# Kernel tuning notes

Measured on AMD Instinct MI355X. Metric: run time of the kernel, lower is better.

## Reference

```python
import jax, jax.numpy as jnp
import numpy as np

EPS = 1e-5
NUM_HEADS = 16
HEAD_DIM = 64


def layernorm(x, g, b):
    mu = jnp.mean(x, axis=-1, keepdims=True)
    var = jnp.mean(jnp.square(x - mu), axis=-1, keepdims=True)
    return (x - mu) * jax.lax.rsqrt(var + EPS) * g + b


def setup_inputs() -> dict:
    key = jax.random.key(0)
    ks = jax.random.split(key, 10)
    B, S, Q, D = 4, 4096, 256, 1024
    x = jax.random.normal(ks[0], (B, S, D), dtype=jnp.float32)
    queries = jax.random.normal(ks[1], (B, Q, D), dtype=jnp.float32)
    attn_mask = jax.random.randint(ks[2], (B, NUM_HEADS, Q, S), 0, 2) == 1
    key_padding_mask = jax.random.randint(ks[3], (B, S), 0, 2) == 1
    scale = 1.0 / np.sqrt(2.0 * D)  # xavier-ish
    Wq = jax.random.normal(ks[4], (D, D), dtype=jnp.float32) * scale
    Wk = jax.random.normal(ks[5], (D, D), dtype=jnp.float32) * scale
    Wv = jax.random.normal(ks[6], (D, D), dtype=jnp.float32) * scale
    Wo = jax.random.normal(ks[7], (D, D), dtype=jnp.float32) * scale
    ln1_g = jnp.ones((D,), jnp.float32); ln1_b = jnp.zeros((D,), jnp.float32)
    ln2_g = jnp.ones((D,), jnp.float32); ln2_b = jnp.zeros((D,), jnp.float32)
    return {"x": x, "queries": queries, "attn_mask": attn_mask,
            "key_padding_mask": key_padding_mask, "Wq": Wq, "Wk": Wk,
            "Wv": Wv, "Wo": Wo, "ln1_g": ln1_g, "ln1_b": ln1_b,
            "ln2_g": ln2_g, "ln2_b": ln2_b}


def reference(x, queries, attn_mask, key_padding_mask, Wq, Wk, Wv, Wo,
              ln1_g, ln1_b, ln2_g, ln2_b):
    B, S, D = x.shape
    Q = queries.shape[1]
    H, hd = NUM_HEADS, HEAD_DIM

    xn = layernorm(x, ln1_g, ln1_b)
    q = (queries @ Wq.T).reshape(B, Q, H, hd)
    k = (xn @ Wk.T).reshape(B, S, H, hd)
    v = (xn @ Wv.T).reshape(B, S, H, hd)

    # scores: (B, H, Q, S)
    scores = jnp.einsum('bqhd,bshd->bhqs', q, k) / np.sqrt(hd)

    mask = attn_mask | key_padding_mask[:, None, None, :]
    neg_inf = jnp.float32(-jnp.inf)
    masked = jnp.where(mask, neg_inf, scores)
    all_masked = jnp.all(mask, axis=-1, keepdims=True)  # rows fully masked
    safe = jnp.where(all_masked, 0.0, masked)
    attn = jax.nn.softmax(safe, axis=-1)
    attn = jnp.where(all_masked, 0.0, attn)

    out = jnp.einsum('bhqs,bshd->bqhd', attn, v).reshape(B, Q, D)
    out = layernorm(out, ln2_g, ln2_b)
    return out @ Wo.T, attn.mean(axis=1)
```

## Files before the change

### kernel.cpp

```cpp
#include <hip/hip_runtime.h>
#include <math.h>

#define DEV __device__ __forceinline__

typedef float  f4v  __attribute__((ext_vector_type(4)));
typedef __bf16 b8v  __attribute__((ext_vector_type(8)));
typedef short  s8v  __attribute__((ext_vector_type(8)));

DEV short f2b(float f){ __bf16 h = (__bf16)f; return __builtin_bit_cast(short, h); }
DEV float b2f(short s){ __bf16 h = __builtin_bit_cast(__bf16, s); return (float)h; }

DEV void gload16(const void* g, void* l){
  __builtin_amdgcn_global_load_lds((const __attribute__((address_space(1))) void*)g,
                                   (__attribute__((address_space(3))) void*)l, 16, 0, 0);
}

DEV b8v ldsf(const short* p){ return __builtin_bit_cast(b8v, *(const s8v*)p); }

DEV f4v mfma16(b8v a, b8v b, f4v c){ return __builtin_amdgcn_mfma_f32_16x16x32_bf16(a, b, c, 0, 0, 0); }

DEV void lds_barrier(){
  asm volatile("s_waitcnt lgkmcnt(0)" ::: "memory");
  __builtin_amdgcn_s_barrier();
}

__global__ __launch_bounds__(256) void prep_kernel(const float* __restrict__ x, const float* __restrict__ ln1g,
                                                   const float* __restrict__ ln1b, short* __restrict__ xn,
                                                   const float* __restrict__ s0, const float* __restrict__ s1,
                                                   const float* __restrict__ s2, const float* __restrict__ s3,
                                                   const float* __restrict__ s4,
                                                   short* __restrict__ d0, short* __restrict__ d1,
                                                   short* __restrict__ d2, short* __restrict__ d3,
                                                   short* __restrict__ d4){
  int bid = blockIdx.x, tid = threadIdx.x;
  if (bid < 5120){
    int i = bid*256 + tid;
    int buf = i >> 18, j = i & 262143;
    const float* s = (buf==0)?s0:(buf==1)?s1:(buf==2)?s2:(buf==3)?s3:s4;
    short*       d = (buf==0)?d0:(buf==1)?d1:(buf==2)?d2:(buf==3)?d3:d4;
    float4 v = ((const float4*)s)[j];
    ((short4*)d)[j] = make_short4(f2b(v.x), f2b(v.y), f2b(v.z), f2b(v.w));
    return;
  }
  int row = bid - 5120;
  const float4 v = ((const float4*)(x + (size_t)row*1024))[tid];
  float s = v.x + v.y + v.z + v.w;
  #pragma unroll
  for (int off=1; off<64; off<<=1) s += __shfl_xor(s, off);
  __shared__ float red[4];
  if ((tid&63)==0) red[tid>>6] = s;
  __syncthreads();
  float mu = (red[0]+red[1]+red[2]+red[3]) * (1.0f/1024.0f);
  float e0=v.x-mu, e1=v.y-mu, e2=v.z-mu, e3=v.w-mu;
  float q = e0*e0 + e1*e1 + e2*e2 + e3*e3;
  #pragma unroll
  for (int off=1; off<64; off<<=1) q += __shfl_xor(q, off);
  __syncthreads();
  if ((tid&63)==0) red[tid>>6] = q;
  __syncthreads();
  float rs = rsqrtf((red[0]+red[1]+red[2]+red[3]) * (1.0f/1024.0f) + 1e-5f);
  float4 g4 = ((const float4*)ln1g)[tid];
  float4 b4 = ((const float4*)ln1b)[tid];
  short4 o = make_short4(f2b(e0*rs*g4.x + b4.x), f2b(e1*rs*g4.y + b4.y),
                         f2b(e2*rs*g4.z + b4.z), f2b(e3*rs*g4.w + b4.w));
  ((short4*)(xn + (size_t)row*1024))[tid] = o;
}

__global__ __launch_bounds__(256) void ln_reduce_kernel(const short* __restrict__ opart, const float* __restrict__ gg,
                                                        const float* __restrict__ bb, short* __restrict__ out){
  int row = blockIdx.x, tid = threadIdx.x;
  float a0=0.f, a1=0.f, a2=0.f, a3=0.f;
  #pragma unroll
  for (int sc=0; sc<16; ++sc){
    short4 t = ((const short4*)(opart + ((size_t)sc*1024 + row)*1024))[tid];
    a0 += b2f(t.x); a1 += b2f(t.y); a2 += b2f(t.z); a3 += b2f(t.w);
  }
  float s = a0 + a1 + a2 + a3;
  #pragma unroll
  for (int off=1; off<64; off<<=1) s += __shfl_xor(s, off);
  __shared__ float red[4];
  if ((tid&63)==0) red[tid>>6] = s;
  __syncthreads();
  float mu = (red[0]+red[1]+red[2]+red[3]) * (1.0f/1024.0f);
  float d0=a0-mu, d1=a1-mu, d2=a2-mu, d3=a3-mu;
  float q = d0*d0 + d1*d1 + d2*d2 + d3*d3;
  #pragma unroll
  for (int off=1; off<64; off<<=1) q += __shfl_xor(q, off);
  __syncthreads();
  if ((tid&63)==0) red[tid>>6] = q;
  __syncthreads();
  float rs = rsqrtf((red[0]+red[1]+red[2]+red[3]) * (1.0f/1024.0f) + 1e-5f);
  float4 g4 = ((const float4*)gg)[tid];
  float4 b4 = ((const float4*)bb)[tid];
  short4 o = make_short4(f2b(d0*rs*g4.x + b4.x), f2b(d1*rs*g4.y + b4.y),
                         f2b(d2*rs*g4.z + b4.z), f2b(d3*rs*g4.w + b4.w));
  ((short4*)(out + (size_t)row*1024))[tid] = o;
}

template<int OUTF32>
__global__ __launch_bounds__(256) void gemm_small(const short* __restrict__ A, const short* __restrict__ B,
                                                  void* __restrict__ C, int M, int N, int K){
  __shared__ short sA[2][64*64];
  __shared__ short sB[2][64*64];
  int tid=threadIdx.x, lane=tid&63, wv=tid>>6, g=lane>>4, r=lane&15;
  int wr=wv>>1, wc=wv&1;
  int m0=blockIdx.x*64, n0=blockIdx.y*64;
  f4v z = {0.f,0.f,0.f,0.f};
  f4v acc[2][2];
  #pragma unroll
  for (int i=0;i<2;++i){
    #pragma unroll
    for (int j=0;j<2;++j) acc[i][j]=z;
  }
  auto stage = [&](int buf, int kt){
    #pragma unroll
    for (int i=0;i<2;++i){
      int idx = i*256 + tid;
      int row = idx>>3, cbs = (idx&7)^(row&7);
      gload16(A + (size_t)(m0+row)*K + kt*64 + cbs*8, &sA[buf][(i*256+wv*64)*8]);
      gload16(B + (size_t)(n0+row)*K + kt*64 + cbs*8, &sB[buf][(i*256+wv*64)*8]);
    }
  };
  int nkt = K >> 6;
  stage(0, 0);
  __syncthreads();
  for (int kt=0; kt<nkt; ++kt){
    int cur = kt & 1;
    if (kt+1 < nkt) stage(cur^1, kt+1);
    b8v af[2][2], bf[2][2];
    #pragma unroll
    for (int mf=0;mf<2;++mf){
      #pragma unroll
      for (int ks=0;ks<2;++ks){
        int ra = wr*32 + mf*16 + r;
        int rb = wc*32 + mf*16 + r;
        af[mf][ks] = ldsf(&sA[cur][ra*64 + (((ks*4+g)^(ra&7))*8)]);
        bf[mf][ks] = ldsf(&sB[cur][rb*64 + (((ks*4+g)^(rb&7))*8)]);
      }
    }
    #pragma unroll
    for (int mf=0;mf<2;++mf){
      #pragma unroll
      for (int nf=0;nf<2;++nf){
        acc[mf][nf] = mfma16(af[mf][0], bf[nf][0], acc[mf][nf]);
        acc[mf][nf] = mfma16(af[mf][1], bf[nf][1], acc[mf][nf]);
      }
    }
    __syncthreads();
  }
  #pragma unroll
  for (int mf=0;mf<2;++mf){
    #pragma unroll
    for (int nf=0;nf<2;++nf){
      #pragma unroll
      for (int j=0;j<4;++j){
        int m = m0 + wr*32 + mf*16 + g*4 + j;
        int n = n0 + wc*32 + nf*16 + r;
        if (OUTF32) ((float*)C)[(size_t)m*N + n] = acc[mf][nf][j];
        else        ((short*)C)[(size_t)m*N + n] = f2b(acc[mf][nf][j]);
      }
    }
  }
}

__global__ __launch_bounds__(512,2) void gemm_dual_bt(const short* __restrict__ A, const short* __restrict__ B0,
                                                      const short* __restrict__ B1, short* __restrict__ C0,
                                                      short* __restrict__ vt, int M, int N, int K){
  __shared__ short sA[2][256*32];
  __shared__ short sB0[2][128*32];
  __shared__ short sB1[2][128*32];
  int tid=threadIdx.x, lane=tid&63, wv=tid>>6, g=lane>>4, r=lane&15;
  int wr=wv>>1, wc=wv&1;
  int m0=blockIdx.x*256, n0=blockIdx.y*128;
  f4v z = {0.f,0.f,0.f,0.f};
  f4v a0[4][4], a1[4][4];
  #pragma unroll
  for (int i=0;i<4;++i){
    #pragma unroll
    for (int j=0;j<4;++j){ a0[i][j]=z; a1[i][j]=z; }
  }
  auto stage = [&](int buf, int kt){
    #pragma unroll
    for (int i=0;i<2;++i){
      int idx = i*512 + tid;
      int row = idx>>2, sl = (idx&3)^(row&3);
      gload16(A + (size_t)(m0+row)*K + kt*32 + sl*8, &sA[buf][(i*512+wv*64)*8]);
    }
    {
      int row = tid>>2, sl = (tid&3)^(row&3);
      gload16(B0 + (size_t)(n0+row)*K + kt*32 + sl*8, &sB0[buf][(wv*64)*8]);
      gload16(B1 + (size_t)(n0+row)*K + kt*32 + sl*8, &sB1[buf][(wv*64)*8]);
    }
  };
  int nkt = K >> 5;
  stage(0, 0);
  __syncthreads();
  for (int kt=0; kt<nkt; ++kt){
    int cur = kt & 1;
    if (kt+1 < nkt) stage(cur^1, kt+1);
    b8v af[4], b0f[4], b1f[4];
    #pragma unroll
    for (int mf=0;mf<4;++mf){
      int ra = wr*64+mf*16+r;
      af[mf] = ldsf(&sA[cur][ra*32 + ((g^(ra&3))*8)]);
    }
    #pragma unroll
    for (int nf=0;nf<4;++nf){
      int rb = wc*64+nf*16+r;
      b0f[nf] = ldsf(&sB0[cur][rb*32 + ((g^(rb&3))*8)]);
      b1f[nf] = ldsf(&sB1[cur][rb*32 + ((g^(rb&3))*8)]);
    }
    #pragma unroll
    for (int mf=0;mf<4;++mf){
      #pragma unroll
      for (int nf=0;nf<4;++nf){
        a0[mf][nf] = mfma16(af[mf], b0f[nf], a0[mf][nf]);
        a1[mf][nf] = mfma16(af[mf], b1f[nf], a1[mf][nf]);
      }
    }
    __syncthreads();
  }
  int b = m0 >> 12;
  #pragma unroll
  for (int mf=0;mf<4;++mf){
    #pragma unroll
    for (int nf=0;nf<4;++nf){
      int m = m0 + wr*64 + mf*16 + g*4;
      int n = n0 + wc*64 + nf*16 + r;
      #pragma unroll
      for (int j=0;j<4;++j)
        C0[(size_t)(m+j)*N + n] = f2b(a0[mf][nf][j]);
      int h = n >> 6, hd = n & 63;
      short4 vv = make_short4(f2b(a1[mf][nf][0]), f2b(a1[mf][nf][1]),
                              f2b(a1[mf][nf][2]), f2b(a1[mf][nf][3]));
      *(short4*)&vt[(size_t)((b*16 + h)*64 + hd)*4096 + (m & 4095)] = vv;
    }
  }
}

__global__ __launch_bounds__(256,2) void lsum_kernel(const short* __restrict__ qp, const short* __restrict__ kb,
                                                     const int* __restrict__ am, const int* __restrict__ kpm,
                                                     unsigned* __restrict__ pm, float* __restrict__ lpart){
  int bid = blockIdx.x;
  int sc = bid & 15, bh = bid >> 4;
  int b = bh >> 4, h = bh & 15;
  int s0 = sc*256;
  __shared__ short sQ[256*64];
  __shared__ short sK[256*64];
  __shared__ unsigned sPM[256*8];
  int tid=threadIdx.x, lane=tid&63, wv=tid>>6, g=lane>>4, r=lane&15;

  #pragma unroll
  for (int i=0;i<8;++i){
    int idx = i*256 + wv*64 + lane;
    int row = idx>>3, cbs = (idx&7)^(row&7);
    gload16(qp + (size_t)(b*256 + row)*1024 + h*64 + cbs*8, &sQ[(i*256+wv*64)*8]);
  }
  #pragma unroll
  for (int i=0;i<8;++i){
    int idx = i*256 + wv*64 + lane;
    int row = idx>>3, cbs = (idx&7)^(row&7);
    gload16(kb + (size_t)(b*4096 + s0 + row)*1024 + h*64 + cbs*8, &sK[(i*256+wv*64)*8]);
  }
  int4 kp = *(const int4*)(kpm + (size_t)b*4096 + s0 + lane*4);
  bool k0 = kp.x!=0, k1 = kp.y!=0, k2 = kp.z!=0, k3 = kp.w!=0;
  #pragma unroll 4
  for (int i=0;i<64;++i){
    int row = wv*64 + i;
    const int4 t = *(const int4*)(am + (size_t)(bh*256 + row)*4096 + s0 + lane*4);
    unsigned long long m0 = __ballot(k0 || (t.x!=0));
    unsigned long long m1 = __ballot(k1 || (t.y!=0));
    unsigned long long m2 = __ballot(k2 || (t.z!=0));
    unsigned long long m3 = __ballot(k3 || (t.w!=0));
    if (lane < 8){
      int jj = lane>>1, hh = lane&1;
      unsigned long long bj = (jj==0)?m0:((jj==1)?m1:((jj==2)?m2:m3));
      unsigned w = (unsigned)(bj >> (hh*32));
      sPM[row*8 + lane] = w;
      pm[(size_t)bid*2048 + row*8 + lane] = w;
    }
  }
  __syncthreads();

  b8v a[4][2];
  #pragma unroll
  for (int mf=0;mf<4;++mf){
    #pragma unroll
    for (int ks=0;ks<2;++ks){
      int q = wv*64 + mf*16 + r;
      a[mf][ks] = ldsf(&sQ[q*64 + (((ks*4+g)^(q&7))*8)]);
    }
  }
  unsigned wmr[4][4][2];
  #pragma unroll
  for (int mf=0;mf<4;++mf){
    #pragma unroll
    for (int jq=0;jq<4;++jq){
      int q = wv*64 + mf*16 + g*4 + jq;
      wmr[mf][jq][0] = sPM[q*8 + (r&3)*2 + 0];
      wmr[mf][jq][1] = sPM[q*8 + (r&3)*2 + 1];
    }
  }
  float lacc[4][4];
  #pragma unroll
  for (int mf=0;mf<4;++mf){
    #pragma unroll
    for (int j=0;j<4;++j) lacc[mf][j] = 0.f;
  }
  f4v z = {0.f,0.f,0.f,0.f};
  #pragma unroll 4
  for (int nf=0;nf<16;++nf){
    int srow = nf*16 + r;
    b8v b0 = ldsf(&sK[srow*64 + ((g^(srow&7))*8)]);
    b8v b1 = ldsf(&sK[srow*64 + (((4+g)^(srow&7))*8)]);
    f4v acc[4];
    #pragma unroll
    for (int mf=0;mf<4;++mf){
      acc[mf] = mfma16(a[mf][0], b0, z);
      acc[mf] = mfma16(a[mf][1], b1, acc[mf]);
    }
    int bitp = 4*(nf&7) + (r>>2);
    #pragma unroll
    for (int mf=0;mf<4;++mf){
      #pragma unroll
      for (int j=0;j<4;++j){
        bool mskd = (wmr[mf][j][nf>>3] >> bitp) & 1u;
        lacc[mf][j] += mskd ? 0.f : __expf(acc[mf][j]*0.125f);
      }
    }
  }
  #pragma unroll
  for (int off=1; off<16; off<<=1){
    #pragma unroll
    for (int mf=0;mf<4;++mf){
      #pragma unroll
      for (int j=0;j<4;++j) lacc[mf][j] += __shfl_xor(lacc[mf][j], off);
    }
  }
  if (r == 0){
    #pragma unroll
    for (int mf=0;mf<4;++mf){
      #pragma unroll
      for (int j=0;j<4;++j){
        int q = wv*64 + mf*16 + g*4 + j;
        lpart[(size_t)bid*256 + q] = lacc[mf][j];
      }
    }
  }
}

__global__ void lcomb_kernel(const float* __restrict__ lpart, float* __restrict__ linv){
  int row = blockIdx.x*256 + threadIdx.x;
  int q = row & 255, bh = row >> 8;
  float l = 0.f;
  #pragma unroll
  for (int sc=0; sc<16; ++sc) l += lpart[(size_t)(bh*16+sc)*256 + q];
  linv[row] = (l > 0.f) ? (1.0f/l) : 0.f;
}

__global__ __launch_bounds__(512,2) void attn_pv_kernel(const short* __restrict__ qp, const short* __restrict__ kb,
                                                        const short* __restrict__ vt, const unsigned* __restrict__ pm,
                                                        const float* __restrict__ linv, short* __restrict__ opart,
                                                        float* __restrict__ out2){
  int bid = blockIdx.x;
  int sc = bid & 15, qt = (bid>>4)&3, b = bid>>6;
  int s0 = sc*256, q0 = qt*64;
  __shared__ short sK[2][256*64];
  __shared__ short sV[2][64*256];
  __shared__ short sQ[2][64*64];
  __shared__ unsigned sPM[2][64*8];
  int tid=threadIdx.x, lane=tid&63, wv=tid>>6, g=lane>>4, r=lane&15;
  int wq = wv>>2, ws = wv&3;
  f4v z = {0.f,0.f,0.f,0.f};
  float macc[4][2][4];
  #pragma unroll
  for (int sb=0;sb<4;++sb){
    #pragma unroll
    for (int qb=0;qb<2;++qb){
      #pragma unroll
      for (int j=0;j<4;++j) macc[sb][qb][j] = 0.f;
    }
  }

  auto stage = [&](int buf, int h){
    int bh = b*16 + h;
    { int row = tid>>3, cbs = (tid&7)^(row&7);
      gload16(qp + (size_t)(b*256 + q0 + row)*1024 + h*64 + cbs*8, &sQ[buf][(wv*64)*8]); }
    #pragma unroll
    for (int i=0;i<4;++i){
      int idx = i*512 + tid;
      int row = idx>>3, cbs = (idx&7)^(row&7);
      gload16(kb + (size_t)(b*4096 + s0 + row)*1024 + h*64 + cbs*8, &sK[buf][(i*512+wv*64)*8]);
    }
    #pragma unroll
    for (int i=0;i<4;++i){
      int idx = i*512 + tid;
      int row = idx>>5, sl = idx&31, sls = sl^(row&7);
      gload16(vt + (size_t)(bh*64 + row)*4096 + s0 + sls*8, &sV[buf][(i*512+wv*64)*8]);
    }
  };
  auto pmload = [&](int h)->unsigned {
    return pm[(size_t)((b*16+h)*16+sc)*2048 + (q0 + (tid>>3))*8 + (tid&7)];
  };

  stage(0, 0);
  sPM[0][tid] = pmload(0);
  __syncthreads();

  for (int h=0; h<16; ++h){
    int cur = h&1;
    unsigned pmnext = 0;
    if (h < 15){
      stage(cur^1, h+1);
      pmnext = pmload(h+1);
    }
    int bh = b*16 + h;

    b8v qf[2][2];
    #pragma unroll
    for (int qb=0;qb<2;++qb){
      #pragma unroll
      for (int ks=0;ks<2;++ks){
        int qrow = wq*32 + qb*16 + r;
        qf[qb][ks] = ldsf(&sQ[cur][qrow*64 + (((ks*4+g)^(qrow&7))*8)]);
      }
    }
    f4v accs[4][2];
    __builtin_amdgcn_s_setprio(1);
    #pragma unroll
    for (int sb=0;sb<4;++sb){
      int srow = ws*64 + sb*16 + r;
      b8v k0 = ldsf(&sK[cur][srow*64 + ((g^(srow&7))*8)]);
      b8v k1 = ldsf(&sK[cur][srow*64 + (((4+g)^(srow&7))*8)]);
      #pragma unroll
      for (int qb=0;qb<2;++qb){
        accs[sb][qb] = mfma16(k0, qf[qb][0], z);
        accs[sb][qb] = mfma16(k1, qf[qb][1], accs[sb][qb]);
      }
    }
    __builtin_amdgcn_s_setprio(0);
    lds_barrier();

    float iv[2];
    iv[0] = linv[(size_t)bh*256 + q0 + wq*32 + r];
    iv[1] = linv[(size_t)bh*256 + q0 + wq*32 + 16 + r];
    unsigned wmq[2][4];
    #pragma unroll
    for (int qb=0;qb<2;++qb){
      #pragma unroll
      for (int j=0;j<4;++j)
        wmq[qb][j] = sPM[cur][(wq*32+qb*16+r)*8 + j*2 + (ws>>1)];
    }
    short* P = &sK[cur][0];
    #pragma unroll
    for (int sb=0;sb<4;++sb){
      int bitp = (ws&1)*16 + sb*4 + g;
      #pragma unroll
      for (int qb=0;qb<2;++qb){
        float pj[4];
        #pragma unroll
        for (int j=0;j<4;++j){
          bool mskd = (wmq[qb][j] >> bitp) & 1u;
          pj[j] = mskd ? 0.f : __expf(accs[sb][qb][j]*0.125f) * iv[qb];
          macc[sb][qb][j] += pj[j];
        }
        int q = wq*32 + qb*16 + r;
        unsigned lo = ((unsigned)(unsigned short)f2b(pj[0])) | (((unsigned)(unsigned short)f2b(pj[1]))<<16);
        unsigned hi = ((unsigned)(unsigned short)f2b(pj[2])) | (((unsigned)(unsigned short)f2b(pj[3]))<<16);
        int sbase = (ws*64 + sb*16 + g*4) ^ ((q&7)<<3);
        uint2 pk; pk.x = lo; pk.y = hi;
        *(uint2*)&P[q*256 + sbase] = pk;
      }
    }
    lds_barrier();

    f4v acco[2]; acco[0]=z; acco[1]=z;
    __builtin_amdgcn_s_setprio(1);
    #pragma unroll
    for (int ks=0;ks<8;++ks){
      int vrow = ws*16 + r;
      b8v bv = ldsf(&sV[cur][vrow*256 + (((ks*4+g)^(vrow&7))*8)]);
      #pragma unroll
      for (int mf=0;mf<2;++mf){
        int prow = wq*32 + mf*16 + r;
        b8v ap = ldsf(&P[prow*256 + ((ks*32+g*8) ^ ((prow&7)<<3))]);
        acco[mf] = mfma16(ap, bv, acco[mf]);
      }
    }
    __builtin_amdgcn_s_setprio(0);
    #pragma unroll
    for (int mf=0;mf<2;++mf){
      #pragma unroll
      for (int j=0;j<4;++j)
        opart[((size_t)sc*1024 + b*256 + q0 + wq*32 + mf*16 + g*4 + j)*1024 + h*64 + ws*16 + r] = f2b(acco[mf][j]);
    }
    if (h < 15) sPM[cur^1][tid] = pmnext;
    __syncthreads();
  }

  #pragma unroll
  for (int sb=0;sb<4;++sb){
    #pragma unroll
    for (int qb=0;qb<2;++qb){
      int q = q0 + wq*32 + qb*16 + r;
      float4 o = make_float4(macc[sb][qb][0]*0.0625f, macc[sb][qb][1]*0.0625f,
                             macc[sb][qb][2]*0.0625f, macc[sb][qb][3]*0.0625f);
      *(float4*)&out2[(size_t)(b*256 + q)*4096 + s0 + ws*64 + sb*16 + g*4] = o;
    }
  }
}

extern "C" void kernel_launch(void* const* d_in, const int* in_sizes, int n_in,
                              void* d_out, int out_size, void* d_ws, size_t ws_size,
                              hipStream_t stream){
  const float* x       = (const float*)d_in[0];
  const float* queries = (const float*)d_in[1];
  const int*   am      = (const int*)d_in[2];
  const int*   kpm     = (const int*)d_in[3];
  const float* Wq      = (const float*)d_in[4];
  const float* Wk      = (const float*)d_in[5];
  const float* Wv      = (const float*)d_in[6];
  const float* Wo      = (const float*)d_in[7];
  const float* ln1g    = (const float*)d_in[8];
  const float* ln1b    = (const float*)d_in[9];
  const float* ln2g    = (const float*)d_in[10];
  const float* ln2b    = (const float*)d_in[11];
  float* out0 = (float*)d_out;
  float* out2 = out0 + (size_t)4*256*1024;
  char* ws = (char*)d_ws;

  size_t off = 0;
  auto alloc = [&](size_t bytes){ void* p = ws + off; off += (bytes + 255) & ~(size_t)255; return p; };
  short*    xn   = (short*)alloc(33554432);
  short*    kb   = (short*)alloc(33554432);
  short*    vt   = (short*)alloc(33554432);
  short*    wqb  = (short*)alloc(2097152);
  short*    wkb  = (short*)alloc(2097152);
  short*    wvb  = (short*)alloc(2097152);
  short*    wob  = (short*)alloc(2097152);
  short*    qbf  = (short*)alloc(2097152);
  short*    qpj  = (short*)alloc(2097152);
  unsigned* pmw  = (unsigned*)alloc(8388608);
  float*    lpart= (float*)alloc(1048576);
  float*    linv = (float*)alloc(65536);
  short*    opart= (short*)alloc(33554432);
  short*    onb  = (short*)alloc(2097152);

  prep_kernel<<<21504,256,0,stream>>>(x, ln1g, ln1b, xn,
                                      queries, Wq, Wk, Wv, Wo, qbf, wqb, wkb, wvb, wob);
  gemm_dual_bt<<<dim3(64,8),512,0,stream>>>(xn, wkb, wvb, kb, vt, 16384, 1024, 1024);
  gemm_small<0><<<dim3(16,16),256,0,stream>>>(qbf, wqb, qpj, 1024, 1024, 1024);
  lsum_kernel<<<1024,256,0,stream>>>(qpj, kb, am, kpm, pmw, lpart);
  lcomb_kernel<<<64,256,0,stream>>>(lpart, linv);
  attn_pv_kernel<<<256,512,0,stream>>>(qpj, kb, vt, pmw, linv, opart, out2);
  ln_reduce_kernel<<<1024,256,0,stream>>>(opart, ln2g, ln2b, onb);
  gemm_small<1><<<dim3(16,16),256,0,stream>>>(onb, wob, out0, 1024, 1024, 1024);
}
```

Baseline: 328.5 us.

## Split attention PV kernel into 128-key chunks with single-buffered LDS

After: 323.1 us. Within noise of the previous version (-1.6%).

```diff
diff --git a/kernel.cpp b/kernel.cpp
--- a/kernel.cpp
+++ b/kernel.cpp
@@ -71,7 +71,7 @@
   int row = blockIdx.x, tid = threadIdx.x;
   float a0=0.f, a1=0.f, a2=0.f, a3=0.f;
   #pragma unroll
-  for (int sc=0; sc<16; ++sc){
+  for (int sc=0; sc<32; ++sc){
     short4 t = ((const short4*)(opart + ((size_t)sc*1024 + row)*1024))[tid];
     a0 += b2f(t.x); a1 += b2f(t.y); a2 += b2f(t.z); a3 += b2f(t.w);
   }
@@ -358,23 +358,24 @@
   linv[row] = (l > 0.f) ? (1.0f/l) : 0.f;
 }
 
-__global__ __launch_bounds__(512,2) void attn_pv_kernel(const short* __restrict__ qp, const short* __restrict__ kb,
+__global__ __launch_bounds__(512,4) void attn_pv_kernel(const short* __restrict__ qp, const short* __restrict__ kb,
                                                         const short* __restrict__ vt, const unsigned* __restrict__ pm,
                                                         const float* __restrict__ linv, short* __restrict__ opart,
                                                         float* __restrict__ out2){
   int bid = blockIdx.x;
-  int sc = bid & 15, qt = (bid>>4)&3, b = bid>>6;
-  int s0 = sc*256, q0 = qt*64;
-  __shared__ short sK[2][256*64];
-  __shared__ short sV[2][64*256];
-  __shared__ short sQ[2][64*64];
-  __shared__ unsigned sPM[2][64*8];
+  int sc = bid & 31, qt = (bid>>5)&3, b = bid>>7;
+  int s0 = sc*128, q0 = qt*64;
+  int half = sc & 1, scq = sc >> 1;
+  __shared__ short sK[128*64];
+  __shared__ short sV[64*128];
+  __shared__ short sQ[64*64];
+  __shared__ unsigned sPM[64*4];
   int tid=threadIdx.x, lane=tid&63, wv=tid>>6, g=lane>>4, r=lane&15;
   int wq = wv>>2, ws = wv&3;
   f4v z = {0.f,0.f,0.f,0.f};
-  float macc[4][2][4];
-  #pragma unroll
-  for (int sb=0;sb<4;++sb){
+  float macc[2][2][4];
+  #pragma unroll
+  for (int sb=0;sb<2;++sb){
     #pragma unroll
     for (int qb=0;qb<2;++qb){
       #pragma unroll
@@ -382,39 +383,25 @@
     }
   }
 
-  auto stage = [&](int buf, int h){
+  for (int h=0; h<16; ++h){
     int bh = b*16 + h;
     { int row = tid>>3, cbs = (tid&7)^(row&7);
-      gload16(qp + (size_t)(b*256 + q0 + row)*1024 + h*64 + cbs*8, &sQ[buf][(wv*64)*8]); }
-    #pragma unroll
-    for (int i=0;i<4;++i){
+      gload16(qp + (size_t)(b*256 + q0 + row)*1024 + h*64 + cbs*8, &sQ[(wv*64)*8]); }
+    #pragma unroll
+    for (int i=0;i<2;++i){
       int idx = i*512 + tid;
       int row = idx>>3, cbs = (idx&7)^(row&7);
-      gload16(kb + (size_t)(b*4096 + s0 + row)*1024 + h*64 + cbs*8, &sK[buf][(i*512+wv*64)*8]);
-    }
-    #pragma unroll
-    for (int i=0;i<4;++i){
+      gload16(kb + (size_t)(b*4096 + s0 + row)*1024 + h*64 + cbs*8, &sK[(i*512+wv*64)*8]);
+    }
+    #pragma unroll
+    for (int i=0;i<2;++i){
       int idx = i*512 + tid;
-      int row = idx>>5, sl = idx&31, sls = sl^(row&7);
-      gload16(vt + (size_t)(bh*64 + row)*4096 + s0 + sls*8, &sV[buf][(i*512+wv*64)*8]);
-    }
-  };
-  auto pmload = [&](int h)->unsigned {
-    return pm[(size_t)((b*16+h)*16+sc)*2048 + (q0 + (tid>>3))*8 + (tid&7)];
-  };
-
-  stage(0, 0);
-  sPM[0][tid] = pmload(0);
-  __syncthreads();
-
-  for (int h=0; h<16; ++h){
-    int cur = h&1;
-    unsigned pmnext = 0;
-    if (h < 15){
-      stage(cur^1, h+1);
-      pmnext = pmload(h+1);
-    }
-    int bh = b*16 + h;
+      int row = idx>>4, sl = idx&15, sls = sl^(row&7);
+      gload16(vt + (size_t)(bh*64 + row)*4096 + s0 + sls*8, &sV[(i*512+wv*64)*8]);
+    }
+    if (tid < 256)
+      sPM[tid] = pm[(size_t)(bh*16+scq)*2048 + (q0 + (tid>>2))*8 + (tid&3)*2 + half];
+    __syncthreads();
 
     b8v qf[2][2];
     #pragma unroll
@@ -422,16 +409,16 @@
       #pragma unroll
       for (int ks=0;ks<2;++ks){
         int qrow = wq*32 + qb*16 + r;
-        qf[qb][ks] = ldsf(&sQ[cur][qrow*64 + (((ks*4+g)^(qrow&7))*8)]);
-      }
-    }
-    f4v accs[4][2];
+        qf[qb][ks] = ldsf(&sQ[qrow*64 + (((ks*4+g)^(qrow&7))*8)]);
+      }
+    }
+    f4v accs[2][2];
     __builtin_amdgcn_s_setprio(1);
     #pragma unroll
-    for (int sb=0;sb<4;++sb){
-      int srow = ws*64 + sb*16 + r;
-      b8v k0 = ldsf(&sK[cur][srow*64 + ((g^(srow&7))*8)]);
-      b8v k1 = ldsf(&sK[cur][srow*64 + (((4+g)^(srow&7))*8)]);
+    for (int sb=0;sb<2;++sb){
+      int srow = ws*32 + sb*16 + r;
+      b8v k0 = ldsf(&sK[srow*64 + ((g^(srow&7))*8)]);
+      b8v k1 = ldsf(&sK[srow*64 + (((4+g)^(srow&7))*8)]);
       #pragma unroll
       for (int qb=0;qb<2;++qb){
         accs[sb][qb] = mfma16(k0, qf[qb][0], z);
@@ -449,12 +436,12 @@
     for (int qb=0;qb<2;++qb){
       #pragma unroll
       for (int j=0;j<4;++j)
-        wmq[qb][j] = sPM[cur][(wq*32+qb*16+r)*8 + j*2 + (ws>>1)];
-    }
-    short* P = &sK[cur][0];
-    #pragma unroll
-    for (int sb=0;sb<4;++sb){
-      int bitp = (ws&1)*16 + sb*4 + g;
+        wmq[qb][j] = sPM[(wq*32+qb*16+r)*4 + j];
+    }
+    short* P = &sK[0];
+    #pragma unroll
+    for (int sb=0;sb<2;++sb){
+      int bitp = ws*8 + sb*4 + g;
       #pragma unroll
       for (int qb=0;qb<2;++qb){
         float pj[4];
@@ -467,9 +454,9 @@
         int q = wq*32 + qb*16 + r;
         unsigned lo = ((unsigned)(unsigned short)f2b(pj[0])) | (((unsigned)(unsigned short)f2b(pj[1]))<<16);
         unsigned hi = ((unsigned)(unsigned short)f2b(pj[2])) | (((unsigned)(unsigned short)f2b(pj[3]))<<16);
-        int sbase = (ws*64 + sb*16 + g*4) ^ ((q&7)<<3);
+        int sbase = (ws*32 + sb*16 + g*4) ^ ((q&7)<<3);
         uint2 pk; pk.x = lo; pk.y = hi;
-        *(uint2*)&P[q*256 + sbase] = pk;
+        *(uint2*)&P[q*128 + sbase] = pk;
       }
     }
     lds_barrier();
@@ -477,13 +464,13 @@
     f4v acco[2]; acco[0]=z; acco[1]=z;
     __builtin_amdgcn_s_setprio(1);
     #pragma unroll
-    for (int ks=0;ks<8;++ks){
+    for (int ks=0;ks<4;++ks){
       int vrow = ws*16 + r;
-      b8v bv = ldsf(&sV[cur][vrow*256 + (((ks*4+g)^(vrow&7))*8)]);
+      b8v bv = ldsf(&sV[vrow*128 + ((ks*32+g*8) ^ ((vrow&7)<<3))]);
       #pragma unroll
       for (int mf=0;mf<2;++mf){
         int prow = wq*32 + mf*16 + r;
-        b8v ap = ldsf(&P[prow*256 + ((ks*32+g*8) ^ ((prow&7)<<3))]);
+        b8v ap = ldsf(&P[prow*128 + ((ks*32+g*8) ^ ((prow&7)<<3))]);
         acco[mf] = mfma16(ap, bv, acco[mf]);
       }
     }
@@ -494,18 +481,17 @@
       for (int j=0;j<4;++j)
         opart[((size_t)sc*1024 + b*256 + q0 + wq*32 + mf*16 + g*4 + j)*1024 + h*64 + ws*16 + r] = f2b(acco[mf][j]);
     }
-    if (h < 15) sPM[cur^1][tid] = pmnext;
-    __syncthreads();
-  }
-
-  #pragma unroll
-  for (int sb=0;sb<4;++sb){
+    lds_barrier();
+  }
+
+  #pragma unroll
+  for (int sb=0;sb<2;++sb){
     #pragma unroll
     for (int qb=0;qb<2;++qb){
       int q = q0 + wq*32 + qb*16 + r;
       float4 o = make_float4(macc[sb][qb][0]*0.0625f, macc[sb][qb][1]*0.0625f,
                              macc[sb][qb][2]*0.0625f, macc[sb][qb][3]*0.0625f);
-      *(float4*)&out2[(size_t)(b*256 + q)*4096 + s0 + ws*64 + sb*16 + g*4] = o;
+      *(float4*)&out2[(size_t)(b*256 + q)*4096 + s0 + ws*32 + sb*16 + g*4] = o;
     }
   }
 }
@@ -543,7 +529,7 @@
   unsigned* pmw  = (unsigned*)alloc(8388608);
   float*    lpart= (float*)alloc(1048576);
   float*    linv = (float*)alloc(65536);
-  short*    opart= (short*)alloc(33554432);
+  short*    opart= (short*)alloc(67108864);
   short*    onb  = (short*)alloc(2097152);
 
   prep_kernel<<<21504,256,0,stream>>>(x, ln1g, ln1b, xn,
@@ -552,7 +538,7 @@
   gemm_small<0><<<dim3(16,16),256,0,stream>>>(qbf, wqb, qpj, 1024, 1024, 1024);
   lsum_kernel<<<1024,256,0,stream>>>(qpj, kb, am, kpm, pmw, lpart);
   lcomb_kernel<<<64,256,0,stream>>>(lpart, linv);
-  attn_pv_kernel<<<256,512,0,stream>>>(qpj, kb, vt, pmw, linv, opart, out2);
+  attn_pv_kernel<<<512,512,0,stream>>>(qpj, kb, vt, pmw, linv, opart, out2);
   ln_reduce_kernel<<<1024,256,0,stream>>>(opart, ln2g, ln2b, onb);
   gemm_small<1><<<dim3(16,16),256,0,stream>>>(onb, wob, out0, 1024, 1024, 1024);
 }
```
